# Kernel optimization log

Hardware: AMD Instinct MI355X
Metric: run time of the kernel (lower is better)

Reference implementation:

```python
import jax, jax.numpy as jnp
import numpy as np

T, L, N, DR = 8, 8, 500, 32
D = 2 * DR          # dr2 = 64
K = 12              # neighbors per region
S = 2               # number_sp attention layers


def setup_inputs() -> dict:
    key = jax.random.key(0)
    ks = jax.random.split(key, 14)
    inp = {}
    inp["all_data_static"] = jax.random.normal(ks[0], (T, L, N, D), jnp.float32)
    inp["thre_nc"] = jax.random.uniform(ks[1], (T, L, N, 1), jnp.float32)
    inp["all_data_dynamic_now"] = jax.random.uniform(ks[2], (L, N, D), jnp.float32)
    inp["neigh_poi"] = jax.random.randint(ks[3], (N, K), 0, N)
    inp["neigh_road"] = jax.random.randint(ks[4], (N, K), 0, N)
    inp["neigh_record"] = jax.random.randint(ks[5], (N, K), 0, N)
    inp["w1"] = jax.random.normal(ks[6], (2 * D, D), jnp.float32) * 0.05
    inp["wq_all"] = jax.random.normal(ks[7], (2, 3, S, D, D), jnp.float32) * 0.05
    inp["wk_all"] = jax.random.normal(ks[8], (2, 3, S, D, D), jnp.float32) * 0.05
    inp["wd_all"] = jax.random.normal(ks[9], (2, 3, S, D, D), jnp.float32) * 0.05
    inp["wmix_all"] = jax.random.normal(ks[10], (2, 3, D), jnp.float32) * 0.1
    inp["conv_w"] = jax.random.normal(ks[11], (4, 2 * D + 1), jnp.float32) * 0.05
    inp["conv_b"] = jnp.zeros((4,), jnp.float32)
    inp["fin_w"] = jax.random.normal(ks[12], (N, N), jnp.float32) * 0.02
    inp["fin_b"] = jnp.ones((N,), jnp.float32)
    return inp


def _attention(data, neigh, wq, wk, wd):
    # data: (T,L,N,D), neigh: (N,K)
    dn = data[:, :, neigh, :]                                   # (T,L,N,K,D) gather
    q = jnp.einsum('tlnd,de->tlne', data, wq)                   # (T,L,N,D)
    k = jnp.einsum('tlnkd,de->tlnke', dn, wk)                   # (T,L,N,K,D)
    a = jax.nn.softmax(jnp.einsum('tlne,tlnke->tlnk', q, k), -1)
    out = q + jnp.einsum('tlnk,tlnke->tlne', a, k)              # residual on q
    return jax.nn.sigmoid(jnp.einsum('tlnd,de->tlne', out, wd))


def _multiattention(data, neighs, wq, wk, wd, wmix):
    outs = []
    for g in range(3):  # poi, road, record
        x = data
        for s in range(wq.shape[1]):
            x = _attention(x, neighs[g], wq[g, s], wk[g, s], wd[g, s])
        outs.append(x)
    return jax.nn.sigmoid(outs[0] * wmix[0] + outs[1] * wmix[1] + outs[2] * wmix[2])


def reference(all_data_static, thre_nc, all_data_dynamic_now,
              neigh_poi, neigh_road, neigh_record,
              w1, wq_all, wk_all, wd_all, wmix_all,
              conv_w, conv_b, fin_w, fin_b):
    # --- Evolution: gated recurrence over time steps 1..T-1 ---
    def evo_step(now, xs):
        st, th = xs  # (L,N,D), (L,N,1)
        new = jax.nn.sigmoid(jnp.concatenate([now, st], -1) @ w1 * th
                             + now * (1.0 - th))
        return new, (new, new - now)
    now_final, (dyn_rest, diffs) = jax.lax.scan(
        evo_step, all_data_dynamic_now, (all_data_static[1:], thre_nc[1:]))
    all_dyn = jnp.concatenate([all_data_dynamic_now[None], dyn_rest], 0)  # (T,L,N,D)

    neighs = (neigh_poi, neigh_road, neigh_record)
    dyn = _multiattention(all_dyn, neighs, wq_all[0], wk_all[0], wd_all[0], wmix_all[0])
    sta = _multiattention(all_data_static, neighs, wq_all[1], wk_all[1], wd_all[1], wmix_all[1])
    x = jnp.concatenate([dyn, sta], -1)                          # (T,L,N,2D)

    # --- ConvLSTM, kernel (1,1), hidden_dim=1 -> pointwise gated recurrence ---
    h0 = jnp.zeros((x.shape[0], x.shape[2], 1), x.dtype)         # (T,N,1)
    def cell(carry, xt):  # xt: (T,N,2D)
        h, c = carry
        gates = jnp.concatenate([xt, h], -1) @ conv_w.T + conv_b  # (T,N,4)
        i = jax.nn.sigmoid(gates[..., 0:1])
        f = jax.nn.sigmoid(gates[..., 1:2])
        o = jax.nn.sigmoid(gates[..., 2:3])
        g = jnp.tanh(gates[..., 3:4])
        c2 = f * c + i * g
        h2 = o * jnp.tanh(c2)
        return (h2, c2), None
    (h_last, _), _ = jax.lax.scan(cell, (h0, h0), jnp.swapaxes(x, 0, 1))

    out = jax.nn.sigmoid(h_last[..., 0] @ fin_w.T + fin_b)       # (T,N)
    return out, now_final, diffs
```

## Files before the change

kernel.cpp:

```cpp
#include <hip/hip_runtime.h>
#include <math.h>

namespace {
constexpr int kT = 8, kL = 8, kN = 500, kD = 64, kK = 12;
constexpr int kLN  = kL * kN;
constexpr int kTLN = kT * kL * kN;
constexpr int kBUF = kTLN * kD;
constexpr int XS = 68;
}

__device__ __forceinline__ float sigf(float v) { return 1.f / (1.f + __expf(-v)); }

__device__ __forceinline__ void stage_x(const float* __restrict__ src, float* lds,
                                        int row0, int M) {
    int r  = threadIdx.x >> 4;
    int c4 = (threadIdx.x & 15) << 2;
#pragma unroll
    for (int i = 0; i < 4; ++i) {
        int rr  = r + 16 * i;
        int row = row0 + rr;
        row = row < M ? row : M - 1;
        float4 v = *reinterpret_cast<const float4*>(src + (size_t)row * 64 + c4);
        *reinterpret_cast<float4*>(lds + rr * XS + c4) = v;
    }
}

template <int K>
__device__ __forceinline__ void stage_w(const float* __restrict__ w, float* lds) {
    const float4* s = reinterpret_cast<const float4*>(w);
    float4* d = reinterpret_cast<float4*>(lds);
#pragma unroll
    for (int i = 0; i < K / 16; ++i)
        d[threadIdx.x + 256 * i] = s[threadIdx.x + 256 * i];
}

__device__ __forceinline__ void gemm_core(const float* ldsx, const float* ldsw,
                                          int rblk, int cblk, float4 acc[4]) {
#pragma unroll 4
    for (int k = 0; k < 64; k += 4) {
        float4 xv[4], wv[4];
#pragma unroll
        for (int i = 0; i < 4; ++i)
            xv[i] = *reinterpret_cast<const float4*>(ldsx + (4 * rblk + i) * XS + k);
#pragma unroll
        for (int d = 0; d < 4; ++d)
            wv[d] = *reinterpret_cast<const float4*>(ldsw + (k + d) * 64 + 4 * cblk);
#pragma unroll
        for (int i = 0; i < 4; ++i) {
            float xs[4] = {xv[i].x, xv[i].y, xv[i].z, xv[i].w};
#pragma unroll
            for (int d = 0; d < 4; ++d) {
                acc[i].x = fmaf(xs[d], wv[d].x, acc[i].x);
                acc[i].y = fmaf(xs[d], wv[d].y, acc[i].y);
                acc[i].z = fmaf(xs[d], wv[d].z, acc[i].z);
                acc[i].w = fmaf(xs[d], wv[d].w, acc[i].w);
            }
        }
    }
}

__device__ __forceinline__ void gemm_core_gw(const float* ldsx,
                                             const float* __restrict__ gw,
                                             int rblk, int cblk, float4 acc[4]) {
#pragma unroll 4
    for (int k = 0; k < 64; k += 4) {
        float4 xv[4], wv[4];
#pragma unroll
        for (int i = 0; i < 4; ++i)
            xv[i] = *reinterpret_cast<const float4*>(ldsx + (4 * rblk + i) * XS + k);
#pragma unroll
        for (int d = 0; d < 4; ++d)
            wv[d] = *reinterpret_cast<const float4*>(gw + (k + d) * 64 + 4 * cblk);
#pragma unroll
        for (int i = 0; i < 4; ++i) {
            float xs[4] = {xv[i].x, xv[i].y, xv[i].z, xv[i].w};
#pragma unroll
            for (int d = 0; d < 4; ++d) {
                acc[i].x = fmaf(xs[d], wv[d].x, acc[i].x);
                acc[i].y = fmaf(xs[d], wv[d].y, acc[i].y);
                acc[i].z = fmaf(xs[d], wv[d].z, acc[i].z);
                acc[i].w = fmaf(xs[d], wv[d].w, acc[i].w);
            }
        }
    }
}

__device__ __forceinline__ void gemm_core2(const float* ldsx, const float* ldswa,
                                           const float* ldswb, int rblk, int cblk,
                                           float4 acca[4], float4 accb[4]) {
#pragma unroll 4
    for (int k = 0; k < 64; k += 4) {
        float4 xv[4], wa[4], wb[4];
#pragma unroll
        for (int i = 0; i < 4; ++i)
            xv[i] = *reinterpret_cast<const float4*>(ldsx + (4 * rblk + i) * XS + k);
#pragma unroll
        for (int d = 0; d < 4; ++d) {
            wa[d] = *reinterpret_cast<const float4*>(ldswa + (k + d) * 64 + 4 * cblk);
            wb[d] = *reinterpret_cast<const float4*>(ldswb + (k + d) * 64 + 4 * cblk);
        }
#pragma unroll
        for (int i = 0; i < 4; ++i) {
            float xs[4] = {xv[i].x, xv[i].y, xv[i].z, xv[i].w};
#pragma unroll
            for (int d = 0; d < 4; ++d) {
                acca[i].x = fmaf(xs[d], wa[d].x, acca[i].x);
                acca[i].y = fmaf(xs[d], wa[d].y, acca[i].y);
                acca[i].z = fmaf(xs[d], wa[d].z, acca[i].z);
                acca[i].w = fmaf(xs[d], wa[d].w, acca[i].w);
                accb[i].x = fmaf(xs[d], wb[d].x, accb[i].x);
                accb[i].y = fmaf(xs[d], wb[d].y, accb[i].y);
                accb[i].z = fmaf(xs[d], wb[d].z, accb[i].z);
                accb[i].w = fmaf(xs[d], wb[d].w, accb[i].w);
            }
        }
    }
}

__device__ __forceinline__ void gemm_core2_gw(const float* ldsx,
                                              const float* __restrict__ gwa,
                                              const float* __restrict__ gwb,
                                              int rblk, int cblk,
                                              float4 acca[4], float4 accb[4]) {
#pragma unroll 4
    for (int k = 0; k < 64; k += 4) {
        float4 xv[4], wa[4], wb[4];
#pragma unroll
        for (int i = 0; i < 4; ++i)
            xv[i] = *reinterpret_cast<const float4*>(ldsx + (4 * rblk + i) * XS + k);
#pragma unroll
        for (int d = 0; d < 4; ++d) {
            wa[d] = *reinterpret_cast<const float4*>(gwa + (k + d) * 64 + 4 * cblk);
            wb[d] = *reinterpret_cast<const float4*>(gwb + (k + d) * 64 + 4 * cblk);
        }
#pragma unroll
        for (int i = 0; i < 4; ++i) {
            float xs[4] = {xv[i].x, xv[i].y, xv[i].z, xv[i].w};
#pragma unroll
            for (int d = 0; d < 4; ++d) {
                acca[i].x = fmaf(xs[d], wa[d].x, acca[i].x);
                acca[i].y = fmaf(xs[d], wa[d].y, acca[i].y);
                acca[i].z = fmaf(xs[d], wa[d].z, acca[i].z);
                acca[i].w = fmaf(xs[d], wa[d].w, acca[i].w);
                accb[i].x = fmaf(xs[d], wb[d].x, accb[i].x);
                accb[i].y = fmaf(xs[d], wb[d].y, accb[i].y);
                accb[i].z = fmaf(xs[d], wb[d].z, accb[i].z);
                accb[i].w = fmaf(xs[d], wb[d].w, accb[i].w);
            }
        }
    }
}

__global__ void __launch_bounds__(256) evo_all_kernel(const float* __restrict__ stat,
                                                      const float* __restrict__ thre,
                                                      const float* __restrict__ dyn0,
                                                      float* __restrict__ all_dyn,
                                                      float* __restrict__ diff,
                                                      float* __restrict__ now_final,
                                                      const float* __restrict__ w1) {
    __shared__ float ldsn[64 * XS];
    __shared__ float ldss[64 * XS];
    __shared__ float ldsw[128 * 64];
    int row0 = blockIdx.x * 64;
    stage_x(dyn0, ldsn, row0, kLN);
    stage_w<128>(w1, ldsw);
    int rblk = threadIdx.x >> 4, cblk = threadIdx.x & 15;
    __syncthreads();
#pragma unroll
    for (int i = 0; i < 4; ++i) {
        int row = row0 + 4 * rblk + i;
        if (row < kLN) {
            float4 x0 = *reinterpret_cast<const float4*>(ldsn + (4 * rblk + i) * XS + 4 * cblk);
            *reinterpret_cast<float4*>(all_dyn + (size_t)row * 64 + 4 * cblk) = x0;
        }
    }
#pragma unroll 1
    for (int t = 1; t < kT; ++t) {
        stage_x(stat + (size_t)t * kLN * kD, ldss, row0, kLN);
        __syncthreads();
        float4 acc[4] = {};
        gemm_core(ldsn, ldsw, rblk, cblk, acc);
        gemm_core(ldss, ldsw + 64 * 64, rblk, cblk, acc);
        float4 nv[4];
#pragma unroll
        for (int i = 0; i < 4; ++i) {
            int row = row0 + 4 * rblk + i;
            int rc  = row < kLN ? row : kLN - 1;
            float tt = thre[t * kLN + rc];
            float4 xn = *reinterpret_cast<const float4*>(ldsn + (4 * rblk + i) * XS + 4 * cblk);
            nv[i].x = sigf(acc[i].x * tt + xn.x * (1.f - tt));
            nv[i].y = sigf(acc[i].y * tt + xn.y * (1.f - tt));
            nv[i].z = sigf(acc[i].z * tt + xn.z * (1.f - tt));
            nv[i].w = sigf(acc[i].w * tt + xn.w * (1.f - tt));
            if (row < kLN) {
                float4 df;
                df.x = nv[i].x - xn.x; df.y = nv[i].y - xn.y;
                df.z = nv[i].z - xn.z; df.w = nv[i].w - xn.w;
                *reinterpret_cast<float4*>(all_dyn + ((size_t)t * kLN + row) * 64 + 4 * cblk) = nv[i];
                *reinterpret_cast<float4*>(diff + ((size_t)(t - 1) * kLN + row) * 64 + 4 * cblk) = df;
                if (t == kT - 1)
                    *reinterpret_cast<float4*>(now_final + (size_t)row * 64 + 4 * cblk) = nv[i];
            }
        }
        __syncthreads();
#pragma unroll
        for (int i = 0; i < 4; ++i)
            *reinterpret_cast<float4*>(ldsn + (4 * rblk + i) * XS + 4 * cblk) = nv[i];
    }
}

__global__ void __launch_bounds__(256) gemm_qk(const float* __restrict__ Xdyn,
                                               const float* __restrict__ Xstat,
                                               const float* __restrict__ wq_all,
                                               const float* __restrict__ wk_all,
                                               float* __restrict__ b1,
                                               float* __restrict__ b2, int step) {
    __shared__ float ldsx[64 * XS];
    __shared__ float ldswq[64 * 64];
    __shared__ float ldswk[64 * 64];
    int c = blockIdx.y;
    int m = c / 3;
    float* b1c = b1 + (size_t)c * kBUF;
    float* b2c = b2 + (size_t)c * kBUF;
    const float* X = step ? b1c : (m == 0 ? Xdyn : Xstat);
    size_t woff = (size_t)(c * 2 + step) * kD * kD;
    int row0 = blockIdx.x * 64;
    stage_x(X, ldsx, row0, kTLN);
    stage_w<64>(wq_all + woff, ldswq);
    stage_w<64>(wk_all + woff, ldswk);
    __syncthreads();
    int rblk = threadIdx.x >> 4, cblk = threadIdx.x & 15;
    float4 aq[4] = {}, ak[4] = {};
    gemm_core2(ldsx, ldswq, ldswk, rblk, cblk, aq, ak);
#pragma unroll
    for (int i = 0; i < 4; ++i) {
        size_t row = row0 + 4 * rblk + i;
        *reinterpret_cast<float4*>(b1c + row * 64 + 4 * cblk) = aq[i];
        *reinterpret_cast<float4*>(b2c + row * 64 + 4 * cblk) = ak[i];
    }
}

__global__ void __launch_bounds__(256) scorewd_kernel(float* __restrict__ b1,
                                                      const float* __restrict__ kbuf,
                                                      const int* __restrict__ npoi,
                                                      const int* __restrict__ nroad,
                                                      const int* __restrict__ nrec,
                                                      const float* __restrict__ wd_all,
                                                      int step) {
    __shared__ float ldsx[64 * XS];
    int p   = blockIdx.y * gridDim.x + blockIdx.x;
    int xcd = p & 7;
    int gid = xcd * 375 + (p >> 3);
    int c    = gid / 500;
    int tile = gid - c * 500;
    int g = c % 3;
    float* b1c = b1 + (size_t)c * kBUF;
    const float* b2c = kbuf + (size_t)c * kBUF;
    const int* neigh = (g == 0) ? npoi : (g == 1) ? nroad : nrec;
    const float* gw = wd_all + (size_t)(c * 2 + step) * kD * kD;

    int lane = threadIdx.x & 63;
    int wv   = threadIdx.x >> 6;
    int sub  = lane >> 4;
    int gq   = lane & 15;
    int row0 = tile * 64;
#pragma unroll 1
    for (int pp = 0; pp < 4; ++pp) {
        int lr  = pp * 16 + wv * 4 + sub;
        int row = row0 + lr;
        int n   = row % kN;
        int slab = row - n;
        float4 q = *(reinterpret_cast<const float4*>(b1c) + (size_t)row * 16 + gq);
        const int4* nbp = reinterpret_cast<const int4*>(neigh + n * kK);
        int4 nb0 = nbp[0], nb1 = nbp[1], nb2 = nbp[2];
        int nb[12] = {nb0.x, nb0.y, nb0.z, nb0.w, nb1.x, nb1.y, nb1.z, nb1.w,
                      nb2.x, nb2.y, nb2.z, nb2.w};
        float4 kv[12];
        float sc[12];
#pragma unroll
        for (int j = 0; j < 12; ++j) {
            kv[j] = *(reinterpret_cast<const float4*>(b2c) + (size_t)(slab + nb[j]) * 16 + gq);
            sc[j] = q.x * kv[j].x + q.y * kv[j].y + q.z * kv[j].z + q.w * kv[j].w;
        }
#pragma unroll
        for (int off = 1; off < 16; off <<= 1) {
#pragma unroll
            for (int j = 0; j < 12; ++j) sc[j] += __shfl_xor(sc[j], off, 16);
        }
        float mx = sc[0];
#pragma unroll
        for (int j = 1; j < 12; ++j) mx = fmaxf(mx, sc[j]);
        float ssum = 0.f;
#pragma unroll
        for (int j = 0; j < 12; ++j) { sc[j] = __expf(sc[j] - mx); ssum += sc[j]; }
        float inv = 1.f / ssum;
        float4 o = q;
#pragma unroll
        for (int j = 0; j < 12; ++j) {
            float a = sc[j] * inv;
            o.x = fmaf(a, kv[j].x, o.x);
            o.y = fmaf(a, kv[j].y, o.y);
            o.z = fmaf(a, kv[j].z, o.z);
            o.w = fmaf(a, kv[j].w, o.w);
        }
        *reinterpret_cast<float4*>(ldsx + lr * XS + 4 * gq) = o;
    }
    __syncthreads();
    int rblk = threadIdx.x >> 4, cblk = threadIdx.x & 15;
    float4 acc[4] = {};
    gemm_core_gw(ldsx, gw, rblk, cblk, acc);
#pragma unroll
    for (int i = 0; i < 4; ++i) {
        size_t idx = ((size_t)(row0 + 4 * rblk + i)) * 64 + 4 * cblk;
        float4 y;
        y.x = sigf(acc[i].x); y.y = sigf(acc[i].y);
        y.z = sigf(acc[i].z); y.w = sigf(acc[i].w);
        *reinterpret_cast<float4*>(b1c + idx) = y;
    }
}

__global__ void __launch_bounds__(256) scorewd_qk_fused(float* __restrict__ b1,
                                                        const float* __restrict__ b2,
                                                        float* __restrict__ b3,
                                                        const int* __restrict__ npoi,
                                                        const int* __restrict__ nroad,
                                                        const int* __restrict__ nrec,
                                                        const float* __restrict__ wd_all,
                                                        const float* __restrict__ wq_all,
                                                        const float* __restrict__ wk_all) {
    __shared__ float ldsx[64 * XS];
    int p   = blockIdx.y * gridDim.x + blockIdx.x;
    int xcd = p & 7;
    int gid = xcd * 375 + (p >> 3);
    int c    = gid / 500;
    int tile = gid - c * 500;
    int g = c % 3;
    float* b1c = b1 + (size_t)c * kBUF;
    const float* b2c = b2 + (size_t)c * kBUF;
    float* b3c = b3 + (size_t)c * kBUF;
    const int* neigh = (g == 0) ? npoi : (g == 1) ? nroad : nrec;
    const float* gwd = wd_all + (size_t)(c * 2 + 0) * kD * kD;
    const float* gwq = wq_all + (size_t)(c * 2 + 1) * kD * kD;
    const float* gwk = wk_all + (size_t)(c * 2 + 1) * kD * kD;

    int lane = threadIdx.x & 63;
    int wv   = threadIdx.x >> 6;
    int sub  = lane >> 4;
    int gq   = lane & 15;
    int row0 = tile * 64;
#pragma unroll 1
    for (int pp = 0; pp < 4; ++pp) {
        int lr  = pp * 16 + wv * 4 + sub;
        int row = row0 + lr;
        int n   = row % kN;
        int slab = row - n;
        float4 q = *(reinterpret_cast<const float4*>(b1c) + (size_t)row * 16 + gq);
        const int4* nbp = reinterpret_cast<const int4*>(neigh + n * kK);
        int4 nb0 = nbp[0], nb1 = nbp[1], nb2 = nbp[2];
        int nb[12] = {nb0.x, nb0.y, nb0.z, nb0.w, nb1.x, nb1.y, nb1.z, nb1.w,
                      nb2.x, nb2.y, nb2.z, nb2.w};
        float4 kv[12];
        float sc[12];
#pragma unroll
        for (int j = 0; j < 12; ++j) {
            kv[j] = *(reinterpret_cast<const float4*>(b2c) + (size_t)(slab + nb[j]) * 16 + gq);
            sc[j] = q.x * kv[j].x + q.y * kv[j].y + q.z * kv[j].z + q.w * kv[j].w;
        }
#pragma unroll
        for (int off = 1; off < 16; off <<= 1) {
#pragma unroll
            for (int j = 0; j < 12; ++j) sc[j] += __shfl_xor(sc[j], off, 16);
        }
        float mx = sc[0];
#pragma unroll
        for (int j = 1; j < 12; ++j) mx = fmaxf(mx, sc[j]);
        float ssum = 0.f;
#pragma unroll
        for (int j = 0; j < 12; ++j) { sc[j] = __expf(sc[j] - mx); ssum += sc[j]; }
        float inv = 1.f / ssum;
        float4 o = q;
#pragma unroll
        for (int j = 0; j < 12; ++j) {
            float a = sc[j] * inv;
            o.x = fmaf(a, kv[j].x, o.x);
            o.y = fmaf(a, kv[j].y, o.y);
            o.z = fmaf(a, kv[j].z, o.z);
            o.w = fmaf(a, kv[j].w, o.w);
        }
        *reinterpret_cast<float4*>(ldsx + lr * XS + 4 * gq) = o;
    }
    __syncthreads();
    int rblk = threadIdx.x >> 4, cblk = threadIdx.x & 15;
    float4 acc[4] = {};
    gemm_core_gw(ldsx, gwd, rblk, cblk, acc);
    float4 y[4];
#pragma unroll
    for (int i = 0; i < 4; ++i) {
        y[i].x = sigf(acc[i].x); y[i].y = sigf(acc[i].y);
        y[i].z = sigf(acc[i].z); y[i].w = sigf(acc[i].w);
    }
    __syncthreads();
#pragma unroll
    for (int i = 0; i < 4; ++i)
        *reinterpret_cast<float4*>(ldsx + (4 * rblk + i) * XS + 4 * cblk) = y[i];
    __syncthreads();
    float4 aq[4] = {}, ak[4] = {};
    gemm_core2_gw(ldsx, gwq, gwk, rblk, cblk, aq, ak);
#pragma unroll
    for (int i = 0; i < 4; ++i) {
        size_t idx = ((size_t)(row0 + 4 * rblk + i)) * 64 + 4 * cblk;
        *reinterpret_cast<float4*>(b1c + idx) = aq[i];
        *reinterpret_cast<float4*>(b3c + idx) = ak[i];
    }
}

__global__ void __launch_bounds__(256) lstm_kernel(const float* __restrict__ b1,
                                                   const float* __restrict__ wmix,
                                                   const float* __restrict__ cw,
                                                   const float* __restrict__ cb,
                                                   float* __restrict__ hlast) {
    int lane = threadIdx.x & 63;
    int wv   = threadIdx.x >> 6;
    int sub  = lane >> 4;
    int fq   = lane & 15;
    int cell = blockIdx.x * 16 + wv * 4 + sub;
    int t = cell / kN, n = cell % kN;
    float wd_[4][4], ws_[4][4], wh[4], bb[4];
#pragma unroll
    for (int gg = 0; gg < 4; ++gg) {
#pragma unroll
        for (int k = 0; k < 4; ++k) {
            wd_[gg][k] = cw[gg * 129 + fq * 4 + k];
            ws_[gg][k] = cw[gg * 129 + 64 + fq * 4 + k];
        }
        wh[gg] = cw[gg * 129 + 128];
        bb[gg] = cb[gg];
    }
    float4 wm[6];
#pragma unroll
    for (int j = 0; j < 6; ++j)
        wm[j] = *reinterpret_cast<const float4*>(wmix + j * 64 + fq * 4);
    float h = 0.f, cc = 0.f;
#pragma unroll 1
    for (int l = 0; l < kL; ++l) {
        size_t row16 = ((size_t)(t * kL + l) * kN + n) * 16 + fq;
        float4 y[6];
#pragma unroll
        for (int j = 0; j < 6; ++j)
            y[j] = *(reinterpret_cast<const float4*>(b1) + (size_t)j * (kBUF / 4) + row16);
        float4 xd, xs;
        xd.x = sigf(y[0].x * wm[0].x + y[1].x * wm[1].x + y[2].x * wm[2].x);
        xd.y = sigf(y[0].y * wm[0].y + y[1].y * wm[1].y + y[2].y * wm[2].y);
        xd.z = sigf(y[0].z * wm[0].z + y[1].z * wm[1].z + y[2].z * wm[2].z);
        xd.w = sigf(y[0].w * wm[0].w + y[1].w * wm[1].w + y[2].w * wm[2].w);
        xs.x = sigf(y[3].x * wm[3].x + y[4].x * wm[4].x + y[5].x * wm[5].x);
        xs.y = sigf(y[3].y * wm[3].y + y[4].y * wm[4].y + y[5].y * wm[5].y);
        xs.z = sigf(y[3].z * wm[3].z + y[4].z * wm[4].z + y[5].z * wm[5].z);
        xs.w = sigf(y[3].w * wm[3].w + y[4].w * wm[4].w + y[5].w * wm[5].w);
        float gsum[4];
#pragma unroll
        for (int gg = 0; gg < 4; ++gg) {
            float v = xd.x * wd_[gg][0] + xd.y * wd_[gg][1]
                    + xd.z * wd_[gg][2] + xd.w * wd_[gg][3];
            v += xs.x * ws_[gg][0] + xs.y * ws_[gg][1]
               + xs.z * ws_[gg][2] + xs.w * ws_[gg][3];
            gsum[gg] = v;
        }
#pragma unroll
        for (int off = 1; off < 16; off <<= 1) {
#pragma unroll
            for (int gg = 0; gg < 4; ++gg) gsum[gg] += __shfl_xor(gsum[gg], off, 16);
        }
        float gi = sigf(gsum[0] + bb[0] + h * wh[0]);
        float gf = sigf(gsum[1] + bb[1] + h * wh[1]);
        float go = sigf(gsum[2] + bb[2] + h * wh[2]);
        float gg_ = tanhf(gsum[3] + bb[3] + h * wh[3]);
        cc = gf * cc + gi * gg_;
        h = go * tanhf(cc);
    }
    if (fq == 0) hlast[cell] = h;
}

__global__ void final_kernel(const float* __restrict__ h, const float* __restrict__ fw,
                             const float* __restrict__ fb, float* __restrict__ out) {
    int wave = threadIdx.x >> 6, lane = threadIdx.x & 63;
    int o = blockIdx.x * 4 + wave;
    int t = o / kN, m = o % kN;
    float acc = 0.f;
    for (int n = lane; n < kN; n += 64)
        acc = fmaf(h[t * kN + n], fw[(size_t)m * kN + n], acc);
#pragma unroll
    for (int off = 32; off > 0; off >>= 1) acc += __shfl_xor(acc, off);
    if (lane == 0) out[o] = sigf(acc + fb[m]);
}

extern "C" void kernel_launch(void* const* d_in, const int* in_sizes, int n_in,
                              void* d_out, int out_size, void* d_ws, size_t ws_size,
                              hipStream_t stream) {
    const float* stat   = (const float*)d_in[0];
    const float* thre   = (const float*)d_in[1];
    const float* dyn0   = (const float*)d_in[2];
    const int*   npoi   = (const int*)d_in[3];
    const int*   nroad  = (const int*)d_in[4];
    const int*   nrec   = (const int*)d_in[5];
    const float* w1     = (const float*)d_in[6];
    const float* wq_all = (const float*)d_in[7];
    const float* wk_all = (const float*)d_in[8];
    const float* wd_all = (const float*)d_in[9];
    const float* wmix   = (const float*)d_in[10];
    const float* conv_w = (const float*)d_in[11];
    const float* conv_b = (const float*)d_in[12];
    const float* fin_w  = (const float*)d_in[13];
    const float* fin_b  = (const float*)d_in[14];

    float* out       = (float*)d_out;
    float* now_final = out + kT * kN;
    float* diffs     = now_final + (size_t)kLN * kD;

    float* ws      = (float*)d_ws;
    float* all_dyn = ws;
    float* b1      = ws + (size_t)kBUF;
    float* b2      = ws + 7 * (size_t)kBUF;

    bool fused = ws_size >= (19 * (size_t)kBUF + (size_t)kT * kN) * sizeof(float);
    float* b3    = ws + 13 * (size_t)kBUF;
    float* hlast = fused ? ws + 19 * (size_t)kBUF
                         : ws + 13 * (size_t)kBUF;

    evo_all_kernel<<<(kLN + 63) / 64, 256, 0, stream>>>(stat, thre, dyn0,
                                                        all_dyn, diffs, now_final, w1);

    dim3 agrid(kTLN / 64, 6);
    gemm_qk<<<agrid, 256, 0, stream>>>(all_dyn, stat, wq_all, wk_all, b1, b2, 0);
    if (fused) {
        scorewd_qk_fused<<<agrid, 256, 0, stream>>>(b1, b2, b3, npoi, nroad, nrec,
                                                    wd_all, wq_all, wk_all);
        scorewd_kernel<<<agrid, 256, 0, stream>>>(b1, b3, npoi, nroad, nrec, wd_all, 1);
    } else {
        scorewd_kernel<<<agrid, 256, 0, stream>>>(b1, b2, npoi, nroad, nrec, wd_all, 0);
        gemm_qk<<<agrid, 256, 0, stream>>>(all_dyn, stat, wq_all, wk_all, b1, b2, 1);
        scorewd_kernel<<<agrid, 256, 0, stream>>>(b1, b2, npoi, nroad, nrec, wd_all, 1);
    }

    lstm_kernel<<<kT * kN / 16, 256, 0, stream>>>(b1, wmix, conv_w, conv_b, hlast);
    final_kernel<<<kT * kN / 4, 256, 0, stream>>>(hlast, fin_w, fin_b, out);
}
```

Measured before the change: 356.3 us.

## Cut register and LDS pressure to raise occupancy in attention kernels

The 12-neighbor gather/softmax is replaced with a chunked online-softmax over three groups of four neighbors, so fewer key vectors stay live in registers. The dual Q/K GEMM is split into two sequential single-weight GEMMs that read weights from global memory, which drops the weight LDS staging in gemm_qk. The kernels also get launch_bounds(256,8) to target higher occupancy. The trade-off is extra rescale exps, serialized gathers and repeated X reads from LDS, plus possible register spills under the tighter bound.

```diff
diff --git a/kernel.cpp b/kernel.cpp
--- a/kernel.cpp
+++ b/kernel.cpp
@@ -85,69 +85,63 @@
     }
 }
 
-__device__ __forceinline__ void gemm_core2(const float* ldsx, const float* ldswa,
-                                           const float* ldswb, int rblk, int cblk,
-                                           float4 acca[4], float4 accb[4]) {
-#pragma unroll 4
-    for (int k = 0; k < 64; k += 4) {
-        float4 xv[4], wa[4], wb[4];
-#pragma unroll
-        for (int i = 0; i < 4; ++i)
-            xv[i] = *reinterpret_cast<const float4*>(ldsx + (4 * rblk + i) * XS + k);
-#pragma unroll
-        for (int d = 0; d < 4; ++d) {
-            wa[d] = *reinterpret_cast<const float4*>(ldswa + (k + d) * 64 + 4 * cblk);
-            wb[d] = *reinterpret_cast<const float4*>(ldswb + (k + d) * 64 + 4 * cblk);
-        }
-#pragma unroll
-        for (int i = 0; i < 4; ++i) {
-            float xs[4] = {xv[i].x, xv[i].y, xv[i].z, xv[i].w};
-#pragma unroll
-            for (int d = 0; d < 4; ++d) {
-                acca[i].x = fmaf(xs[d], wa[d].x, acca[i].x);
-                acca[i].y = fmaf(xs[d], wa[d].y, acca[i].y);
-                acca[i].z = fmaf(xs[d], wa[d].z, acca[i].z);
-                acca[i].w = fmaf(xs[d], wa[d].w, acca[i].w);
-                accb[i].x = fmaf(xs[d], wb[d].x, accb[i].x);
-                accb[i].y = fmaf(xs[d], wb[d].y, accb[i].y);
-                accb[i].z = fmaf(xs[d], wb[d].z, accb[i].z);
-                accb[i].w = fmaf(xs[d], wb[d].w, accb[i].w);
-            }
-        }
-    }
-}
-
-__device__ __forceinline__ void gemm_core2_gw(const float* ldsx,
-                                              const float* __restrict__ gwa,
-                                              const float* __restrict__ gwb,
-                                              int rblk, int cblk,
-                                              float4 acca[4], float4 accb[4]) {
-#pragma unroll 4
-    for (int k = 0; k < 64; k += 4) {
-        float4 xv[4], wa[4], wb[4];
-#pragma unroll
-        for (int i = 0; i < 4; ++i)
-            xv[i] = *reinterpret_cast<const float4*>(ldsx + (4 * rblk + i) * XS + k);
-#pragma unroll
-        for (int d = 0; d < 4; ++d) {
-            wa[d] = *reinterpret_cast<const float4*>(gwa + (k + d) * 64 + 4 * cblk);
-            wb[d] = *reinterpret_cast<const float4*>(gwb + (k + d) * 64 + 4 * cblk);
-        }
-#pragma unroll
-        for (int i = 0; i < 4; ++i) {
-            float xs[4] = {xv[i].x, xv[i].y, xv[i].z, xv[i].w};
-#pragma unroll
-            for (int d = 0; d < 4; ++d) {
-                acca[i].x = fmaf(xs[d], wa[d].x, acca[i].x);
-                acca[i].y = fmaf(xs[d], wa[d].y, acca[i].y);
-                acca[i].z = fmaf(xs[d], wa[d].z, acca[i].z);
-                acca[i].w = fmaf(xs[d], wa[d].w, acca[i].w);
-                accb[i].x = fmaf(xs[d], wb[d].x, accb[i].x);
-                accb[i].y = fmaf(xs[d], wb[d].y, accb[i].y);
-                accb[i].z = fmaf(xs[d], wb[d].z, accb[i].z);
-                accb[i].w = fmaf(xs[d], wb[d].w, accb[i].w);
-            }
-        }
+__device__ __forceinline__ void gather_score_combine(const float* __restrict__ b1c,
+                                                     const float* __restrict__ b2c,
+                                                     const int* __restrict__ neigh,
+                                                     int row0, float* ldsx) {
+    int lane = threadIdx.x & 63;
+    int wv   = threadIdx.x >> 6;
+    int sub  = lane >> 4;
+    int gq   = lane & 15;
+#pragma unroll 1
+    for (int pp = 0; pp < 4; ++pp) {
+        int lr  = pp * 16 + wv * 4 + sub;
+        int row = row0 + lr;
+        int n   = row % kN;
+        int slab = row - n;
+        float4 q = *(reinterpret_cast<const float4*>(b1c) + (size_t)row * 16 + gq);
+        const int4* nbp = reinterpret_cast<const int4*>(neigh + n * kK);
+        float m = -1e30f, s = 0.f;
+        float4 u = {0.f, 0.f, 0.f, 0.f};
+#pragma unroll 1
+        for (int ch = 0; ch < 3; ++ch) {
+            int4 nb = nbp[ch];
+            int nbi[4] = {nb.x, nb.y, nb.z, nb.w};
+            float4 kv[4];
+            float sc[4];
+#pragma unroll
+            for (int j = 0; j < 4; ++j) {
+                kv[j] = *(reinterpret_cast<const float4*>(b2c) + (size_t)(slab + nbi[j]) * 16 + gq);
+                sc[j] = q.x * kv[j].x + q.y * kv[j].y + q.z * kv[j].z + q.w * kv[j].w;
+            }
+#pragma unroll
+            for (int off = 1; off < 16; off <<= 1) {
+#pragma unroll
+                for (int j = 0; j < 4; ++j) sc[j] += __shfl_xor(sc[j], off, 16);
+            }
+            float cm = fmaxf(fmaxf(sc[0], sc[1]), fmaxf(sc[2], sc[3]));
+            float mn = fmaxf(m, cm);
+            float scale = __expf(m - mn);
+            s = s * scale;
+            u.x *= scale; u.y *= scale; u.z *= scale; u.w *= scale;
+#pragma unroll
+            for (int j = 0; j < 4; ++j) {
+                float e = __expf(sc[j] - mn);
+                s += e;
+                u.x = fmaf(e, kv[j].x, u.x);
+                u.y = fmaf(e, kv[j].y, u.y);
+                u.z = fmaf(e, kv[j].z, u.z);
+                u.w = fmaf(e, kv[j].w, u.w);
+            }
+            m = mn;
+        }
+        float inv = 1.f / s;
+        float4 o;
+        o.x = fmaf(u.x, inv, q.x);
+        o.y = fmaf(u.y, inv, q.y);
+        o.z = fmaf(u.z, inv, q.z);
+        o.w = fmaf(u.w, inv, q.w);
+        *reinterpret_cast<float4*>(ldsx + lr * XS + 4 * gq) = o;
     }
 }
 
@@ -209,15 +203,13 @@
     }
 }
 
-__global__ void __launch_bounds__(256) gemm_qk(const float* __restrict__ Xdyn,
-                                               const float* __restrict__ Xstat,
-                                               const float* __restrict__ wq_all,
-                                               const float* __restrict__ wk_all,
-                                               float* __restrict__ b1,
-                                               float* __restrict__ b2, int step) {
+__global__ void __launch_bounds__(256, 8) gemm_qk(const float* __restrict__ Xdyn,
+                                                  const float* __restrict__ Xstat,
+                                                  const float* __restrict__ wq_all,
+                                                  const float* __restrict__ wk_all,
+                                                  float* __restrict__ b1,
+                                                  float* __restrict__ b2, int step) {
     __shared__ float ldsx[64 * XS];
-    __shared__ float ldswq[64 * 64];
-    __shared__ float ldswk[64 * 64];
     int c = blockIdx.y;
     int m = c / 3;
     float* b1c = b1 + (size_t)c * kBUF;
@@ -226,27 +218,31 @@
     size_t woff = (size_t)(c * 2 + step) * kD * kD;
     int row0 = blockIdx.x * 64;
     stage_x(X, ldsx, row0, kTLN);
-    stage_w<64>(wq_all + woff, ldswq);
-    stage_w<64>(wk_all + woff, ldswk);
     __syncthreads();
     int rblk = threadIdx.x >> 4, cblk = threadIdx.x & 15;
-    float4 aq[4] = {}, ak[4] = {};
-    gemm_core2(ldsx, ldswq, ldswk, rblk, cblk, aq, ak);
+    float4 aq[4] = {};
+    gemm_core_gw(ldsx, wq_all + woff, rblk, cblk, aq);
 #pragma unroll
     for (int i = 0; i < 4; ++i) {
         size_t row = row0 + 4 * rblk + i;
         *reinterpret_cast<float4*>(b1c + row * 64 + 4 * cblk) = aq[i];
+    }
+    float4 ak[4] = {};
+    gemm_core_gw(ldsx, wk_all + woff, rblk, cblk, ak);
+#pragma unroll
+    for (int i = 0; i < 4; ++i) {
+        size_t row = row0 + 4 * rblk + i;
         *reinterpret_cast<float4*>(b2c + row * 64 + 4 * cblk) = ak[i];
     }
 }
 
-__global__ void __launch_bounds__(256) scorewd_kernel(float* __restrict__ b1,
-                                                      const float* __restrict__ kbuf,
-                                                      const int* __restrict__ npoi,
-                                                      const int* __restrict__ nroad,
-                                                      const int* __restrict__ nrec,
-                                                      const float* __restrict__ wd_all,
-                                                      int step) {
+__global__ void __launch_bounds__(256, 8) scorewd_kernel(float* __restrict__ b1,
+                                                         const float* __restrict__ kbuf,
+                                                         const int* __restrict__ npoi,
+                                                         const int* __restrict__ nroad,
+                                                         const int* __restrict__ nrec,
+                                                         const float* __restrict__ wd_all,
+                                                         int step) {
     __shared__ float ldsx[64 * XS];
     int p   = blockIdx.y * gridDim.x + blockIdx.x;
     int xcd = p & 7;
@@ -258,53 +254,9 @@
     const float* b2c = kbuf + (size_t)c * kBUF;
     const int* neigh = (g == 0) ? npoi : (g == 1) ? nroad : nrec;
     const float* gw = wd_all + (size_t)(c * 2 + step) * kD * kD;
-
-    int lane = threadIdx.x & 63;
-    int wv   = threadIdx.x >> 6;
-    int sub  = lane >> 4;
-    int gq   = lane & 15;
     int row0 = tile * 64;
-#pragma unroll 1
-    for (int pp = 0; pp < 4; ++pp) {
-        int lr  = pp * 16 + wv * 4 + sub;
-        int row = row0 + lr;
-        int n   = row % kN;
-        int slab = row - n;
-        float4 q = *(reinterpret_cast<const float4*>(b1c) + (size_t)row * 16 + gq);
-        const int4* nbp = reinterpret_cast<const int4*>(neigh + n * kK);
-        int4 nb0 = nbp[0], nb1 = nbp[1], nb2 = nbp[2];
-        int nb[12] = {nb0.x, nb0.y, nb0.z, nb0.w, nb1.x, nb1.y, nb1.z, nb1.w,
-                      nb2.x, nb2.y, nb2.z, nb2.w};
-        float4 kv[12];
-        float sc[12];
-#pragma unroll
-        for (int j = 0; j < 12; ++j) {
-            kv[j] = *(reinterpret_cast<const float4*>(b2c) + (size_t)(slab + nb[j]) * 16 + gq);
-            sc[j] = q.x * kv[j].x + q.y * kv[j].y + q.z * kv[j].z + q.w * kv[j].w;
-        }
-#pragma unroll
-        for (int off = 1; off < 16; off <<= 1) {
-#pragma unroll
-            for (int j = 0; j < 12; ++j) sc[j] += __shfl_xor(sc[j], off, 16);
-        }
-        float mx = sc[0];
-#pragma unroll
-        for (int j = 1; j < 12; ++j) mx = fmaxf(mx, sc[j]);
-        float ssum = 0.f;
-#pragma unroll
-        for (int j = 0; j < 12; ++j) { sc[j] = __expf(sc[j] - mx); ssum += sc[j]; }
-        float inv = 1.f / ssum;
-        float4 o = q;
-#pragma unroll
-        for (int j = 0; j < 12; ++j) {
-            float a = sc[j] * inv;
-            o.x = fmaf(a, kv[j].x, o.x);
-            o.y = fmaf(a, kv[j].y, o.y);
-            o.z = fmaf(a, kv[j].z, o.z);
-            o.w = fmaf(a, kv[j].w, o.w);
-        }
-        *reinterpret_cast<float4*>(ldsx + lr * XS + 4 * gq) = o;
-    }
+
+    gather_score_combine(b1c, b2c, neigh, row0, ldsx);
     __syncthreads();
     int rblk = threadIdx.x >> 4, cblk = threadIdx.x & 15;
     float4 acc[4] = {};
@@ -319,15 +271,15 @@
     }
 }
 
-__global__ void __launch_bounds__(256) scorewd_qk_fused(float* __restrict__ b1,
-                                                        const float* __restrict__ b2,
-                                                        float* __restrict__ b3,
-                                                        const int* __restrict__ npoi,
-                                                        const int* __restrict__ nroad,
-                                                        const int* __restrict__ nrec,
-                                                        const float* __restrict__ wd_all,
-                                                        const float* __restrict__ wq_all,
-                                                        const float* __restrict__ wk_all) {
+__global__ void __launch_bounds__(256, 8) scorewd_qk_fused(float* __restrict__ b1,
+                                                           const float* __restrict__ b2,
+                                                           float* __restrict__ b3,
+                                                           const int* __restrict__ npoi,
+                                                           const int* __restrict__ nroad,
+                                                           const int* __restrict__ nrec,
+                                                           const float* __restrict__ wd_all,
+                                                           const float* __restrict__ wq_all,
+                                                           const float* __restrict__ wk_all) {
     __shared__ float ldsx[64 * XS];
     int p   = blockIdx.y * gridDim.x + blockIdx.x;
     int xcd = p & 7;
@@ -342,53 +294,9 @@
     const float* gwd = wd_all + (size_t)(c * 2 + 0) * kD * kD;
     const float* gwq = wq_all + (size_t)(c * 2 + 1) * kD * kD;
     const float* gwk = wk_all + (size_t)(c * 2 + 1) * kD * kD;
-
-    int lane = threadIdx.x & 63;
-    int wv   = threadIdx.x >> 6;
-    int sub  = lane >> 4;
-    int gq   = lane & 15;
     int row0 = tile * 64;
-#pragma unroll 1
-    for (int pp = 0; pp < 4; ++pp) {
-        int lr  = pp * 16 + wv * 4 + sub;
-        int row = row0 + lr;
-        int n   = row % kN;
-        int slab = row - n;
-        float4 q = *(reinterpret_cast<const float4*>(b1c) + (size_t)row * 16 + gq);
-        const int4* nbp = reinterpret_cast<const int4*>(neigh + n * kK);
-        int4 nb0 = nbp[0], nb1 = nbp[1], nb2 = nbp[2];
-        int nb[12] = {nb0.x, nb0.y, nb0.z, nb0.w, nb1.x, nb1.y, nb1.z, nb1.w,
-                      nb2.x, nb2.y, nb2.z, nb2.w};
-        float4 kv[12];
-        float sc[12];
-#pragma unroll
-        for (int j = 0; j < 12; ++j) {
-            kv[j] = *(reinterpret_cast<const float4*>(b2c) + (size_t)(slab + nb[j]) * 16 + gq);
-            sc[j] = q.x * kv[j].x + q.y * kv[j].y + q.z * kv[j].z + q.w * kv[j].w;
-        }
-#pragma unroll
-        for (int off = 1; off < 16; off <<= 1) {
-#pragma unroll
-            for (int j = 0; j < 12; ++j) sc[j] += __shfl_xor(sc[j], off, 16);
-        }
-        float mx = sc[0];
-#pragma unroll
-        for (int j = 1; j < 12; ++j) mx = fmaxf(mx, sc[j]);
-        float ssum = 0.f;
-#pragma unroll
-        for (int j = 0; j < 12; ++j) { sc[j] = __expf(sc[j] - mx); ssum += sc[j]; }
-        float inv = 1.f / ssum;
-        float4 o = q;
-#pragma unroll
-        for (int j = 0; j < 12; ++j) {
-            float a = sc[j] * inv;
-            o.x = fmaf(a, kv[j].x, o.x);
-            o.y = fmaf(a, kv[j].y, o.y);
-            o.z = fmaf(a, kv[j].z, o.z);
-            o.w = fmaf(a, kv[j].w, o.w);
-        }
-        *reinterpret_cast<float4*>(ldsx + lr * XS + 4 * gq) = o;
-    }
+
+    gather_score_combine(b1c, b2c, neigh, row0, ldsx);
     __syncthreads();
     int rblk = threadIdx.x >> 4, cblk = threadIdx.x & 15;
     float4 acc[4] = {};
@@ -404,12 +312,18 @@
     for (int i = 0; i < 4; ++i)
         *reinterpret_cast<float4*>(ldsx + (4 * rblk + i) * XS + 4 * cblk) = y[i];
     __syncthreads();
-    float4 aq[4] = {}, ak[4] = {};
-    gemm_core2_gw(ldsx, gwq, gwk, rblk, cblk, aq, ak);
+    float4 aq[4] = {};
+    gemm_core_gw(ldsx, gwq, rblk, cblk, aq);
 #pragma unroll
     for (int i = 0; i < 4; ++i) {
         size_t idx = ((size_t)(row0 + 4 * rblk + i)) * 64 + 4 * cblk;
         *reinterpret_cast<float4*>(b1c + idx) = aq[i];
+    }
+    float4 ak[4] = {};
+    gemm_core_gw(ldsx, gwk, rblk, cblk, ak);
+#pragma unroll
+    for (int i = 0; i < 4; ++i) {
+        size_t idx = ((size_t)(row0 + 4 * rblk + i)) * 64 + 4 * cblk;
         *reinterpret_cast<float4*>(b3c + idx) = ak[i];
     }
 }
```

Result: slower. 404.9 us (+13.7%).
